# Optimization experiments

Measured on AMD Instinct MI355X. Metric: run time of the kernel, lower is better.

## Reference

```python
import jax, jax.numpy as jnp
import numpy as np

# Faithful JAX translation of fastmax_function with mask=True, p=1, normalize=0.
# In that branch the torch code sets temperature = 1 and uses a0 = a1 = 1.

def setup_inputs() -> dict:
    key = jax.random.key(0)
    kq, kk, kv = jax.random.split(key, 3)
    b, h, n, d = 2, 8, 8192, 32
    q = jax.random.normal(kq, (b, h, n, d), dtype=jnp.float32)
    k = jax.random.normal(kk, (b, h, n, d), dtype=jnp.float32)
    v = jax.random.normal(kv, (b, h, n, d), dtype=jnp.float32)
    return {"q": q, "k": k, "v": v}


def reference(q, k, v):
    # q, k, v: (b, h, n, d); causal (mask=True), p=1, a0=a1=1, temperature=1
    b, h, n, d = q.shape
    # first term: running sum of values
    first = jnp.cumsum(v, axis=2)                                  # (b,h,n,d)
    # second term: q_i . (sum_{j<=i} k_j v_j^T)
    kv = jnp.einsum('bhnd,bhne->bhnde', k, v)                      # (b,h,n,d,d)
    kv_cs = jnp.cumsum(kv, axis=2)                                 # (b,h,n,d,d)
    second = jnp.einsum('bhnd,bhnde->bhne', q, kv_cs)              # (b,h,n,d)
    # denominator: i + q_i . (sum_{j<=i} k_j)
    k_cs = jnp.cumsum(k, axis=2)                                   # (b,h,n,d)
    div1 = jnp.arange(1, n + 1, dtype=q.dtype)                     # (n,)
    div2 = jnp.einsum('bhnd,bhnd->bhn', q, k_cs)                   # (b,h,n)
    div = (div1[None, None, :] + div2)[..., None]                  # (b,h,n,1)
    return (first + second) / div
```

## Files before the change

kernel.cpp:

```cpp
#include <hip/hip_runtime.h>


#define D      32
#define C      64
#define NCHUNK 128
#define GSIZE  16
#define NGROUP 8
#define BH     16
#define NSEQ   8192
#define STATE  1088

typedef __attribute__((ext_vector_type(8))) short bf16x8;
typedef __attribute__((ext_vector_type(4))) float f32x4;

__device__ __forceinline__ unsigned short f2bf(float x) {
  union { float f; unsigned u; } c; c.f = x;
  unsigned r = (c.u + 0x7FFFu + ((c.u >> 16) & 1u)) >> 16;
  return (unsigned short)r;
}

__global__ __launch_bounds__(256) void chunk_state_kernel(
    const float* __restrict__ k, const float* __restrict__ v,
    float* __restrict__ states) {
  int blk = blockIdx.x;
  int bh  = blk >> 7;
  int c   = blk & 127;
  size_t off = ((size_t)bh * NSEQ + (size_t)c * C) * D;
  const float* kp = k + off;
  const float* vp = v + off;

  __shared__ __align__(16) unsigned short kT[D * 72];
  __shared__ __align__(16) unsigned short vT[D * 72];
  __shared__ __align__(16) float psK[256];
  __shared__ __align__(16) float psV[256];

  int t = threadIdx.x;
  int e = t & 31;
  float sk = 0.f, sv = 0.f;
  for (int r = 0; r < 8; ++r) {
    int idx = t + r * 256;
    int j = idx >> 5;
    float kvv = kp[idx], vvv = vp[idx];
    kT[e * 72 + j] = f2bf(kvv);
    vT[e * 72 + j] = f2bf(vvv);
    sk += kvv; sv += vvv;
  }
  psK[t] = sk; psV[t] = sv;
  __syncthreads();

  int lane = t & 63, w = t >> 6;
  int m16 = lane & 15, quad = lane >> 4;
  int mb = w >> 1, nb = w & 1;
  f32x4 acc = {0.f, 0.f, 0.f, 0.f};
#pragma unroll
  for (int kb = 0; kb < 2; ++kb) {
    bf16x8 a = *(const bf16x8*)&kT[(16 * mb + m16) * 72 + kb * 32 + quad * 8];
    bf16x8 b = *(const bf16x8*)&vT[(16 * nb + m16) * 72 + kb * 32 + quad * 8];
    acc = __builtin_amdgcn_mfma_f32_16x16x32_bf16(a, b, acc, 0, 0, 0);
  }
  float* st = states + (size_t)blk * STATE;
#pragma unroll
  for (int reg = 0; reg < 4; ++reg) {
    int d1 = 16 * mb + quad * 4 + reg;
    int d2 = 16 * nb + m16;
    st[d1 * 32 + d2] = acc[reg];
  }
  if (t < 64) {
    int ee = t & 31;
    float s = 0.f;
    if (t < 32) {
#pragma unroll
      for (int g = 0; g < 8; ++g) s += psK[ee + 32 * g];
      st[1024 + ee] = s;
    } else {
#pragma unroll
      for (int g = 0; g < 8; ++g) s += psV[ee + 32 * g];
      st[1056 + ee] = s;
    }
  }
}

__global__ __launch_bounds__(256) void group_scan_kernel(
    float* __restrict__ states, float* __restrict__ totals) {
  int blk = blockIdx.x;
  float* base = states + (size_t)blk * GSIZE * STATE;
  float* tot  = totals + (size_t)blk * STATE;
  int t = threadIdx.x;
  float a0 = 0.f, a1 = 0.f, a2 = 0.f, a3 = 0.f, a4 = 0.f;
  for (int c = 0; c < GSIZE; ++c) {
    float* p = base + (size_t)c * STATE;
    float s0 = p[t], s1 = p[t + 256], s2 = p[t + 512], s3 = p[t + 768];
    float s4 = (t < 64) ? p[t + 1024] : 0.f;
    p[t] = a0; p[t + 256] = a1; p[t + 512] = a2; p[t + 768] = a3;
    if (t < 64) p[t + 1024] = a4;
    a0 += s0; a1 += s1; a2 += s2; a3 += s3; a4 += s4;
  }
  tot[t] = a0; tot[t + 256] = a1; tot[t + 512] = a2; tot[t + 768] = a3;
  if (t < 64) tot[t + 1024] = a4;
}

__global__ __launch_bounds__(256) void totals_scan_kernel(float* __restrict__ totals) {
  int gidx = blockIdx.x * 256 + threadIdx.x;
  if (gidx >= BH * STATE) return;
  int bh = gidx / STATE;
  int e  = gidx % STATE;
  float* base = totals + (size_t)bh * NGROUP * STATE + e;
  float a = 0.f;
  for (int g = 0; g < NGROUP; ++g) {
    float s = base[(size_t)g * STATE];
    base[(size_t)g * STATE] = a;
    a += s;
  }
}

__global__ __launch_bounds__(256) void output_kernel(
    const float* __restrict__ q, const float* __restrict__ k,
    const float* __restrict__ v, const float* __restrict__ states,
    const float* __restrict__ totals, float* __restrict__ out) {
  int blk = blockIdx.x;
  int bh  = blk >> 7;
  int c   = blk & 127;
  size_t off = ((size_t)bh * NSEQ + (size_t)c * C) * D;
  const float* qp = q + off;
  const float* kp = k + off;
  const float* vp = v + off;
  const float* st  = states + (size_t)blk * STATE;
  const float* tot = totals + ((size_t)(bh * NGROUP + (c >> 4))) * STATE;

  __shared__ __align__(16) unsigned short qbf[C * 40];
  __shared__ __align__(16) unsigned short kbf[C * 40];
  __shared__ __align__(16) unsigned short vTbf[D * 72];
  __shared__ __align__(16) unsigned short kvTbf[D * 40];
  __shared__ __align__(16) unsigned short Tbf[C * 72];
  __shared__ __align__(16) float q_s[C * 36];
  __shared__ __align__(16) float kc_s[C * 36];
  __shared__ __align__(16) float gtot[8 * 32];
  __shared__ __align__(16) float kpre_s[D], vpre_s[D], invdiv_s[C];

  int t = threadIdx.x;
  int e = t & 31;

  for (int z = t; z < (C * 72) / 8; z += 256)
    ((uint4*)Tbf)[z] = make_uint4(0, 0, 0, 0);
  for (int r = 0; r < 8; ++r) {
    int idx = t + r * 256;
    int j = idx >> 5;
    float qv = qp[idx], kv = kp[idx], vv = vp[idx];
    q_s[j * 36 + e]  = qv;  qbf[j * 40 + e] = f2bf(qv);
    kc_s[j * 36 + e] = kv;  kbf[j * 40 + e] = f2bf(kv);
    vTbf[e * 72 + j] = f2bf(vv);
  }
  for (int r = 0; r < 4; ++r) {
    int idx = t + r * 256;
    int dd = idx >> 5;
    kvTbf[e * 40 + dd] = f2bf(st[idx] + tot[idx]);
  }
  if (t < 32)      kpre_s[t]      = st[1024 + t] + tot[1024 + t];
  else if (t < 64) vpre_s[t - 32] = st[1024 + t] + tot[1024 + t];
  __syncthreads();

  int lane = t & 63, w = t >> 6;
  int m16 = lane & 15, quad = lane >> 4;

  const bf16x8 aQ = *(const bf16x8*)&qbf[(16 * w + m16) * 40 + quad * 8];
  for (int jb = 0; jb <= w; ++jb) {
    bf16x8 bK = *(const bf16x8*)&kbf[(16 * jb + m16) * 40 + quad * 8];
    f32x4 cS = {0.f, 0.f, 0.f, 0.f};
    cS = __builtin_amdgcn_mfma_f32_16x16x32_bf16(aQ, bK, cS, 0, 0, 0);
    int jcol = 16 * jb + m16;
#pragma unroll
    for (int reg = 0; reg < 4; ++reg) {
      int i = 16 * w + quad * 4 + reg;
      float tv = (jcol <= i) ? (1.f + cS[reg]) : 0.f;
      Tbf[i * 72 + jcol] = f2bf(tv);
    }
  }
  int rg = t >> 5;
  float vals[8];
  {
    float run = 0.f;
#pragma unroll
    for (int r = 0; r < 8; ++r) {
      vals[r] = kc_s[(rg * 8 + r) * 36 + e];
      run += vals[r];
    }
    gtot[rg * 32 + e] = run;
  }
  __syncthreads();

  {
    float offv = kpre_s[e];
    for (int g = 0; g < rg; ++g) offv += gtot[g * 32 + e];
    float cacc = offv;
#pragma unroll
    for (int r = 0; r < 8; ++r) {
      cacc += vals[r];
      kc_s[(rg * 8 + r) * 36 + e] = cacc;
    }
  }
  __syncthreads();

  if (t < 64) {
    int i = t;
    float dp = 0.f;
#pragma unroll
    for (int d4 = 0; d4 < 8; ++d4) {
      float4 qv = *(const float4*)&q_s[i * 36 + 4 * d4];
      float4 kc = *(const float4*)&kc_s[i * 36 + 4 * d4];
      dp += qv.x * kc.x + qv.y * kc.y + qv.z * kc.z + qv.w * kc.w;
    }
    invdiv_s[i] = 1.f / ((float)(c * C + i + 1) + dp);
  }
  f32x4 o0 = {0.f, 0.f, 0.f, 0.f}, o1 = {0.f, 0.f, 0.f, 0.f};
  {
    bf16x8 b0 = *(const bf16x8*)&kvTbf[(m16)      * 40 + quad * 8];
    bf16x8 b1 = *(const bf16x8*)&kvTbf[(16 + m16) * 40 + quad * 8];
    o0 = __builtin_amdgcn_mfma_f32_16x16x32_bf16(aQ, b0, o0, 0, 0, 0);
    o1 = __builtin_amdgcn_mfma_f32_16x16x32_bf16(aQ, b1, o1, 0, 0, 0);
  }
  int kbcnt = (w >= 2) ? 2 : 1;
  for (int kb = 0; kb < kbcnt; ++kb) {
    bf16x8 aT = *(const bf16x8*)&Tbf[(16 * w + m16) * 72 + kb * 32 + quad * 8];
    bf16x8 b0 = *(const bf16x8*)&vTbf[(m16)      * 72 + kb * 32 + quad * 8];
    bf16x8 b1 = *(const bf16x8*)&vTbf[(16 + m16) * 72 + kb * 32 + quad * 8];
    o0 = __builtin_amdgcn_mfma_f32_16x16x32_bf16(aT, b0, o0, 0, 0, 0);
    o1 = __builtin_amdgcn_mfma_f32_16x16x32_bf16(aT, b1, o1, 0, 0, 0);
  }
  __syncthreads();

#pragma unroll
  for (int reg = 0; reg < 4; ++reg) {
    int i = 16 * w + quad * 4 + reg;
    float id = invdiv_s[i];
    int e0 = m16, e1 = 16 + m16;
    out[off + (size_t)i * D + e0] = (vpre_s[e0] + o0[reg]) * id;
    out[off + (size_t)i * D + e1] = (vpre_s[e1] + o1[reg]) * id;
  }
}

extern "C" void kernel_launch(void* const* d_in, const int* in_sizes, int n_in,
                              void* d_out, int out_size, void* d_ws, size_t ws_size,
                              hipStream_t stream) {
  const float* q = (const float*)d_in[0];
  const float* k = (const float*)d_in[1];
  const float* v = (const float*)d_in[2];
  float* out    = (float*)d_out;
  float* states = (float*)d_ws;
  float* totals = states + (size_t)BH * NCHUNK * STATE;

  chunk_state_kernel<<<BH * NCHUNK, 256, 0, stream>>>(k, v, states);
  group_scan_kernel<<<BH * NGROUP, 256, 0, stream>>>(states, totals);
  totals_scan_kernel<<<(BH * STATE + 255) / 256, 256, 0, stream>>>(totals);
  output_kernel<<<BH * NCHUNK, 256, 0, stream>>>(q, k, v, states, totals, out);
}
```

Baseline: 112.5 us.

## Replace two-level group/totals scan with single batched per-element chunk scan

Drops the two-level scan (group scan plus totals scan) and uses one kernel in which each thread scans one state element across all 128 chunks, loading 16 chunks at a time into registers. The output kernel then reads the fully prefixed state directly, with no totals add. This removes a kernel launch and the extra totals traffic. The cost is a longer serial dependency per thread over only 68 blocks, which may lower parallelism.

```diff
diff --git a/kernel.cpp b/kernel.cpp
--- a/kernel.cpp
+++ b/kernel.cpp
@@ -4,8 +4,6 @@
 #define D      32
 #define C      64
 #define NCHUNK 128
-#define GSIZE  16
-#define NGROUP 8
 #define BH     16
 #define NSEQ   8192
 #define STATE  1088
@@ -80,43 +78,28 @@
   }
 }
 
-__global__ __launch_bounds__(256) void group_scan_kernel(
-    float* __restrict__ states, float* __restrict__ totals) {
-  int blk = blockIdx.x;
-  float* base = states + (size_t)blk * GSIZE * STATE;
-  float* tot  = totals + (size_t)blk * STATE;
-  int t = threadIdx.x;
-  float a0 = 0.f, a1 = 0.f, a2 = 0.f, a3 = 0.f, a4 = 0.f;
-  for (int c = 0; c < GSIZE; ++c) {
-    float* p = base + (size_t)c * STATE;
-    float s0 = p[t], s1 = p[t + 256], s2 = p[t + 512], s3 = p[t + 768];
-    float s4 = (t < 64) ? p[t + 1024] : 0.f;
-    p[t] = a0; p[t + 256] = a1; p[t + 512] = a2; p[t + 768] = a3;
-    if (t < 64) p[t + 1024] = a4;
-    a0 += s0; a1 += s1; a2 += s2; a3 += s3; a4 += s4;
-  }
-  tot[t] = a0; tot[t + 256] = a1; tot[t + 512] = a2; tot[t + 768] = a3;
-  if (t < 64) tot[t + 1024] = a4;
-}
-
-__global__ __launch_bounds__(256) void totals_scan_kernel(float* __restrict__ totals) {
+__global__ __launch_bounds__(256) void scan_kernel(float* __restrict__ states) {
   int gidx = blockIdx.x * 256 + threadIdx.x;
-  if (gidx >= BH * STATE) return;
   int bh = gidx / STATE;
   int e  = gidx % STATE;
-  float* base = totals + (size_t)bh * NGROUP * STATE + e;
+  float* base = states + (size_t)bh * NCHUNK * STATE + e;
   float a = 0.f;
-  for (int g = 0; g < NGROUP; ++g) {
-    float s = base[(size_t)g * STATE];
-    base[(size_t)g * STATE] = a;
-    a += s;
+#pragma unroll 1
+  for (int c0 = 0; c0 < NCHUNK; c0 += 16) {
+    float s[16];
+#pragma unroll
+    for (int r = 0; r < 16; ++r) s[r] = base[(size_t)(c0 + r) * STATE];
+#pragma unroll
+    for (int r = 0; r < 16; ++r) { float tv = s[r]; s[r] = a; a += tv; }
+#pragma unroll
+    for (int r = 0; r < 16; ++r) base[(size_t)(c0 + r) * STATE] = s[r];
   }
 }
 
 __global__ __launch_bounds__(256) void output_kernel(
     const float* __restrict__ q, const float* __restrict__ k,
     const float* __restrict__ v, const float* __restrict__ states,
-    const float* __restrict__ totals, float* __restrict__ out) {
+    float* __restrict__ out) {
   int blk = blockIdx.x;
   int bh  = blk >> 7;
   int c   = blk & 127;
@@ -124,8 +107,7 @@
   const float* qp = q + off;
   const float* kp = k + off;
   const float* vp = v + off;
-  const float* st  = states + (size_t)blk * STATE;
-  const float* tot = totals + ((size_t)(bh * NGROUP + (c >> 4))) * STATE;
+  const float* st = states + (size_t)blk * STATE;
 
   __shared__ __align__(16) unsigned short qbf[C * 40];
   __shared__ __align__(16) unsigned short kbf[C * 40];
@@ -153,10 +135,10 @@
   for (int r = 0; r < 4; ++r) {
     int idx = t + r * 256;
     int dd = idx >> 5;
-    kvTbf[e * 40 + dd] = f2bf(st[idx] + tot[idx]);
-  }
-  if (t < 32)      kpre_s[t]      = st[1024 + t] + tot[1024 + t];
-  else if (t < 64) vpre_s[t - 32] = st[1024 + t] + tot[1024 + t];
+    kvTbf[e * 40 + dd] = f2bf(st[idx]);
+  }
+  if (t < 32)      kpre_s[t]      = st[1024 + t];
+  else if (t < 64) vpre_s[t - 32] = st[1024 + t];
   __syncthreads();
 
   int lane = t & 63, w = t >> 6;
@@ -246,10 +228,8 @@
   const float* v = (const float*)d_in[2];
   float* out    = (float*)d_out;
   float* states = (float*)d_ws;
-  float* totals = states + (size_t)BH * NCHUNK * STATE;
 
   chunk_state_kernel<<<BH * NCHUNK, 256, 0, stream>>>(k, v, states);
-  group_scan_kernel<<<BH * NGROUP, 256, 0, stream>>>(states, totals);
-  totals_scan_kernel<<<(BH * STATE + 255) / 256, 256, 0, stream>>>(totals);
-  output_kernel<<<BH * NCHUNK, 256, 0, stream>>>(q, k, v, states, totals, out);
-}
+  scan_kernel<<<(BH * STATE) / 256, 256, 0, stream>>>(states);
+  output_kernel<<<BH * NCHUNK, 256, 0, stream>>>(q, k, v, states, out);
+}
```

New measurement: 113.3 us. No clear change (+0.7%).
